# Performance work log

Measured on AMD Instinct MI355X. Metric: run time of the kernel, lower is better.

## Reference

```python
import jax, jax.numpy as jnp
import numpy as np

MOMENTUM = 0.1
C_DIM = 5


def setup_inputs() -> dict:
    key = jax.random.key(0)
    k1, k2, k3 = jax.random.split(key, 3)
    B, C, H, W = 16, 256, 128, 128
    im = jax.random.normal(k1, (B, C, H, W), dtype=jnp.float32)
    running_mean = jnp.zeros((2 * C_DIM, C), dtype=jnp.float32)
    running_std = jnp.ones((2 * C_DIM, C), dtype=jnp.float32)
    c_trg = jax.random.randint(k2, (B, C_DIM), 0, 2, dtype=jnp.int32)
    c_org = jax.random.randint(k3, (B, C_DIM), 0, 2, dtype=jnp.int32)
    return {"im": im, "running_mean": running_mean, "running_std": running_std,
            "c_trg": c_trg, "c_org": c_org}


def reference(im, running_mean, running_std, c_trg, c_org):
    B, C, H, W = im.shape
    N = H * W
    # per-sample per-channel instance stats; torch.std_mean uses correction=1
    mean = jnp.mean(im, axis=(2, 3))                      # [B, C]
    var = jnp.sum((im - mean[:, :, None, None]) ** 2, axis=(2, 3)) / (N - 1)
    std = jnp.sqrt(var)                                   # [B, C]

    ct = c_trg.astype(bool)
    co = c_org.astype(bool)
    c_trg_full = jnp.concatenate([ct, ~ct], axis=1)       # [B, 2*c_dim]
    c_org_full = jnp.concatenate([co, ~co], axis=1)       # [B, 2*c_dim]

    m = jnp.float32(MOMENTUM)

    # sequential EMA update of running buffers, in batch order (matches torch loop)
    def step(carry, xs):
        rm, rs = carry
        std_n, mean_n, org_n = xs                         # [C], [C], [2*c_dim]
        msk = org_n[:, None]                              # [2*c_dim, 1]
        rs = jnp.where(msk, rs * (1 - m) + std_n[None, :] * m, rs)
        rm = jnp.where(msk, rm * (1 - m) + mean_n[None, :] * m, rm)
        return (rm, rs), None

    (rm_final, rs_final), _ = jax.lax.scan(
        step, (running_mean, running_std), (std, mean, c_org_full))

    # per-sample gather: mean of selected buffer rows. Exactly c_dim rows are
    # selected per sample (each attribute contributes itself or its negation).
    sel = c_trg_full.astype(im.dtype)                     # [B, 2*c_dim]
    cnt = jnp.sum(sel, axis=1, keepdims=True)             # [B, 1] (== c_dim)
    trg_std = (sel @ rs_final) / cnt                      # [B, C]
    trg_mean = (sel @ rm_final) / cnt                     # [B, C]

    def bc(x):  # [B, C] -> [B, C, 1, 1]
        return x[:, :, None, None]

    return (im - bc(mean)) / bc(std) * bc(trg_std) + bc(trg_mean)
```

## Files before the change

### kernel.cpp

```cpp
#include <hip/hip_runtime.h>
#include <math.h>

#define CDIM 5
constexpr int B_ = 16;
constexpr int C_ = 256;
constexpr int HW_ = 128 * 128;
constexpr float MOM = 0.1f;

constexpr int NSTRIPES = 4;
constexpr int CPS = C_ / NSTRIPES;

using f32x4 = __attribute__((ext_vector_type(4))) float;

__global__ __launch_bounds__(256) void cin_stats(const float* __restrict__ im,
                                                 float* __restrict__ ws_mean,
                                                 float* __restrict__ ws_std,
                                                 int c0) {
    const int ci = blockIdx.x % CPS;
    const int b  = blockIdx.x / CPS;
    const int plane = b * C_ + c0 + ci;

    const f32x4* p4 = (const f32x4*)(im + (size_t)plane * HW_);
    const int t = threadIdx.x;

    float sum = 0.f, sumsq = 0.f;
    #pragma unroll
    for (int it = 0; it < 16; ++it) {
        f32x4 v = p4[it * 256 + t];
        sum   += v.x + v.y + v.z + v.w;
        sumsq += v.x * v.x + v.y * v.y + v.z * v.z + v.w * v.w;
    }

    #pragma unroll
    for (int off = 32; off > 0; off >>= 1) {
        sum   += __shfl_down(sum, off, 64);
        sumsq += __shfl_down(sumsq, off, 64);
    }

    __shared__ float s_sum[4], s_sq[4];
    const int wave = t >> 6;
    if ((t & 63) == 0) { s_sum[wave] = sum; s_sq[wave] = sumsq; }
    __syncthreads();

    if (t == 0) {
        float s = s_sum[0] + s_sum[1] + s_sum[2] + s_sum[3];
        float q = s_sq[0] + s_sq[1] + s_sq[2] + s_sq[3];
        float mean = s / (float)HW_;
        float var = fmaxf(q - s * mean, 0.f) / (float)(HW_ - 1);
        ws_mean[plane] = mean;
        ws_std[plane]  = sqrtf(var);
    }
}

__global__ __launch_bounds__(256) void cin_norm(const float* __restrict__ im,
                                                const float* __restrict__ running_mean,
                                                const float* __restrict__ running_std,
                                                const int* __restrict__ c_trg,
                                                const int* __restrict__ c_org,
                                                const float* __restrict__ ws_mean,
                                                const float* __restrict__ ws_std,
                                                float* __restrict__ out,
                                                int c0) {
    const int ci = blockIdx.x % CPS;
    const int b  = blockIdx.x / CPS;
    const int c  = c0 + ci;
    const int plane = b * C_ + c;

    float rm[2 * CDIM], rs[2 * CDIM];
    #pragma unroll
    for (int r = 0; r < 2 * CDIM; ++r) {
        rm[r] = running_mean[r * C_ + c];
        rs[r] = running_std [r * C_ + c];
    }
    for (int n = 0; n < B_; ++n) {
        const float mn = ws_mean[n * C_ + c];
        const float sd = ws_std [n * C_ + c];
        int bits[CDIM];
        #pragma unroll
        for (int k = 0; k < CDIM; ++k) bits[k] = c_org[n * CDIM + k];
        #pragma unroll
        for (int r = 0; r < 2 * CDIM; ++r) {
            const int k = (r < CDIM) ? r : r - CDIM;
            const bool msk = (r < CDIM) ? (bits[k] != 0) : (bits[k] == 0);
            if (msk) {
                rs[r] = rs[r] * (1.f - MOM) + sd * MOM;
                rm[r] = rm[r] * (1.f - MOM) + mn * MOM;
            }
        }
    }

    float tm = 0.f, ts = 0.f, cnt = 0.f;
    #pragma unroll
    for (int r = 0; r < 2 * CDIM; ++r) {
        const int k = (r < CDIM) ? r : r - CDIM;
        const int bit = c_trg[b * CDIM + k];
        const bool sel = (r < CDIM) ? (bit != 0) : (bit == 0);
        if (sel) { cnt += 1.f; tm += rm[r]; ts += rs[r]; }
    }
    tm /= cnt;
    ts /= cnt;
    const float mean  = ws_mean[plane];
    const float std   = ws_std [plane];
    const float scale = ts / std;
    const float shift = tm - mean * scale;

    const f32x4* p4 = (const f32x4*)(im + (size_t)plane * HW_);
    f32x4*       o4 = (f32x4*)(out + (size_t)plane * HW_);
    const int t = threadIdx.x;

    #pragma unroll
    for (int it = 0; it < 16; ++it) {
        f32x4 v = p4[it * 256 + t];
        f32x4 r;
        r.x = fmaf(v.x, scale, shift);
        r.y = fmaf(v.y, scale, shift);
        r.z = fmaf(v.z, scale, shift);
        r.w = fmaf(v.w, scale, shift);
        __builtin_nontemporal_store(r, &o4[it * 256 + t]);
    }
}

extern "C" void kernel_launch(void* const* d_in, const int* in_sizes, int n_in,
                              void* d_out, int out_size, void* d_ws, size_t ws_size,
                              hipStream_t stream) {
    const float* im           = (const float*)d_in[0];
    const float* running_mean = (const float*)d_in[1];
    const float* running_std  = (const float*)d_in[2];
    const int*   c_trg        = (const int*)d_in[3];
    const int*   c_org        = (const int*)d_in[4];
    float* out = (float*)d_out;

    float* ws      = (float*)d_ws;
    float* ws_mean = ws;
    float* ws_std  = ws + B_ * C_;

    const int blocks = B_ * CPS;

    for (int s = 0; s < NSTRIPES; ++s) {
        const int c0 = s * CPS;
        cin_stats<<<blocks, 256, 0, stream>>>(im, ws_mean, ws_std, c0);
        cin_norm <<<blocks, 256, 0, stream>>>(im, running_mean, running_std,
                                              c_trg, c_org, ws_mean, ws_std,
                                              out, c0);
    }
}
```

Measured before the change: 149.3 us.

## Fuse stats and normalize into one kernel with per-channel atomic barrier

Replaces the striped stats/normalize kernel pairs with a single fused kernel. Each block keeps its plane in registers, publishes its mean and std, then spins on a per-channel atomic counter until all 16 batch entries for that channel are ready. Blocks are ordered channel-major so the 16 blocks of a channel are co-resident. This removes the second read of the input and the extra launches, at the cost of high register pressure and a spin-wait that relies on co-scheduling to avoid deadlock.

```diff
diff --git a/kernel.cpp b/kernel.cpp
--- a/kernel.cpp
+++ b/kernel.cpp
@@ -7,28 +7,39 @@
 constexpr int HW_ = 128 * 128;
 constexpr float MOM = 0.1f;
 
-constexpr int NSTRIPES = 4;
-constexpr int CPS = C_ / NSTRIPES;
-
 using f32x4 = __attribute__((ext_vector_type(4))) float;
 
-__global__ __launch_bounds__(256) void cin_stats(const float* __restrict__ im,
-                                                 float* __restrict__ ws_mean,
-                                                 float* __restrict__ ws_std,
-                                                 int c0) {
-    const int ci = blockIdx.x % CPS;
-    const int b  = blockIdx.x / CPS;
-    const int plane = b * C_ + c0 + ci;
+__global__ __launch_bounds__(256) void cin_zero(int* __restrict__ cnt) {
+    cnt[threadIdx.x] = 0;
+}
+
+__global__ __launch_bounds__(256, 4) void cin_fused(
+        const float* __restrict__ im,
+        const float* __restrict__ running_mean,
+        const float* __restrict__ running_std,
+        const int* __restrict__ c_trg,
+        const int* __restrict__ c_org,
+        float* __restrict__ ws_mean,
+        float* __restrict__ ws_std,
+        int* __restrict__ ws_cnt,
+        float* __restrict__ out) {
+    const int c = blockIdx.x >> 4;
+    const int b = blockIdx.x & 15;
+    const int plane = b * C_ + c;
+    const int t = threadIdx.x;
 
     const f32x4* p4 = (const f32x4*)(im + (size_t)plane * HW_);
-    const int t = threadIdx.x;
+    f32x4 v[16];
+    #pragma unroll
+    for (int it = 0; it < 16; ++it)
+        v[it] = __builtin_nontemporal_load(&p4[it * 256 + t]);
 
     float sum = 0.f, sumsq = 0.f;
     #pragma unroll
     for (int it = 0; it < 16; ++it) {
-        f32x4 v = p4[it * 256 + t];
-        sum   += v.x + v.y + v.z + v.w;
-        sumsq += v.x * v.x + v.y * v.y + v.z * v.z + v.w * v.w;
+        sum   += v[it].x + v[it].y + v[it].z + v[it].w;
+        sumsq += v[it].x * v[it].x + v[it].y * v[it].y
+               + v[it].z * v[it].z + v[it].w * v[it].w;
     }
 
     #pragma unroll
@@ -36,7 +47,6 @@
         sum   += __shfl_down(sum, off, 64);
         sumsq += __shfl_down(sumsq, off, 64);
     }
-
     __shared__ float s_sum[4], s_sq[4];
     const int wave = t >> 6;
     if ((t & 63) == 0) { s_sum[wave] = sum; s_sq[wave] = sumsq; }
@@ -46,25 +56,30 @@
         float s = s_sum[0] + s_sum[1] + s_sum[2] + s_sum[3];
         float q = s_sq[0] + s_sq[1] + s_sq[2] + s_sq[3];
         float mean = s / (float)HW_;
-        float var = fmaxf(q - s * mean, 0.f) / (float)(HW_ - 1);
-        ws_mean[plane] = mean;
-        ws_std[plane]  = sqrtf(var);
+        float var  = fmaxf(q - s * mean, 0.f) / (float)(HW_ - 1);
+        float sd   = sqrtf(var);
+        __hip_atomic_store(&ws_mean[plane], mean, __ATOMIC_RELAXED,
+                           __HIP_MEMORY_SCOPE_AGENT);
+        __hip_atomic_store(&ws_std[plane], sd, __ATOMIC_RELAXED,
+                           __HIP_MEMORY_SCOPE_AGENT);
+        __hip_atomic_fetch_add(&ws_cnt[c], 1, __ATOMIC_RELEASE,
+                               __HIP_MEMORY_SCOPE_AGENT);
+        while (__hip_atomic_load(&ws_cnt[c], __ATOMIC_ACQUIRE,
+                                 __HIP_MEMORY_SCOPE_AGENT) < B_)
+            __builtin_amdgcn_s_sleep(2);
     }
-}
+    __syncthreads();
 
-__global__ __launch_bounds__(256) void cin_norm(const float* __restrict__ im,
-                                                const float* __restrict__ running_mean,
-                                                const float* __restrict__ running_std,
-                                                const int* __restrict__ c_trg,
-                                                const int* __restrict__ c_org,
-                                                const float* __restrict__ ws_mean,
-                                                const float* __restrict__ ws_std,
-                                                float* __restrict__ out,
-                                                int c0) {
-    const int ci = blockIdx.x % CPS;
-    const int b  = blockIdx.x / CPS;
-    const int c  = c0 + ci;
-    const int plane = b * C_ + c;
+    __shared__ float s_mn[B_], s_sd[B_];
+    if (t < B_) {
+        s_mn[t] = __hip_atomic_load(&ws_mean[t * C_ + c], __ATOMIC_RELAXED,
+                                    __HIP_MEMORY_SCOPE_AGENT);
+    } else if (t < 2 * B_) {
+        s_sd[t - B_] = __hip_atomic_load(&ws_std[(t - B_) * C_ + c],
+                                         __ATOMIC_RELAXED,
+                                         __HIP_MEMORY_SCOPE_AGENT);
+    }
+    __syncthreads();
 
     float rm[2 * CDIM], rs[2 * CDIM];
     #pragma unroll
@@ -73,8 +88,8 @@
         rs[r] = running_std [r * C_ + c];
     }
     for (int n = 0; n < B_; ++n) {
-        const float mn = ws_mean[n * C_ + c];
-        const float sd = ws_std [n * C_ + c];
+        const float mn = s_mn[n];
+        const float sd = s_sd[n];
         int bits[CDIM];
         #pragma unroll
         for (int k = 0; k < CDIM; ++k) bits[k] = c_org[n * CDIM + k];
@@ -99,23 +114,19 @@
     }
     tm /= cnt;
     ts /= cnt;
-    const float mean  = ws_mean[plane];
-    const float std   = ws_std [plane];
+    const float mean  = s_mn[b];
+    const float std   = s_sd[b];
     const float scale = ts / std;
     const float shift = tm - mean * scale;
 
-    const f32x4* p4 = (const f32x4*)(im + (size_t)plane * HW_);
-    f32x4*       o4 = (f32x4*)(out + (size_t)plane * HW_);
-    const int t = threadIdx.x;
-
+    f32x4* o4 = (f32x4*)(out + (size_t)plane * HW_);
     #pragma unroll
     for (int it = 0; it < 16; ++it) {
-        f32x4 v = p4[it * 256 + t];
         f32x4 r;
-        r.x = fmaf(v.x, scale, shift);
-        r.y = fmaf(v.y, scale, shift);
-        r.z = fmaf(v.z, scale, shift);
-        r.w = fmaf(v.w, scale, shift);
+        r.x = fmaf(v[it].x, scale, shift);
+        r.y = fmaf(v[it].y, scale, shift);
+        r.z = fmaf(v[it].z, scale, shift);
+        r.w = fmaf(v[it].w, scale, shift);
         __builtin_nontemporal_store(r, &o4[it * 256 + t]);
     }
 }
@@ -133,14 +144,10 @@
     float* ws      = (float*)d_ws;
     float* ws_mean = ws;
     float* ws_std  = ws + B_ * C_;
+    int*   ws_cnt  = (int*)(ws + 2 * B_ * C_);
 
-    const int blocks = B_ * CPS;
-
-    for (int s = 0; s < NSTRIPES; ++s) {
-        const int c0 = s * CPS;
-        cin_stats<<<blocks, 256, 0, stream>>>(im, ws_mean, ws_std, c0);
-        cin_norm <<<blocks, 256, 0, stream>>>(im, running_mean, running_std,
-                                              c_trg, c_org, ws_mean, ws_std,
-                                              out, c0);
-    }
+    cin_zero<<<1, C_, 0, stream>>>(ws_cnt);
+    cin_fused<<<B_ * C_, 256, 0, stream>>>(im, running_mean, running_std,
+                                           c_trg, c_org, ws_mean, ws_std,
+                                           ws_cnt, out);
 }
```

After: 440.0 us. 195% more time.
